# Performance work log

Hardware: AMD Instinct MI355X
Metric: run time of the kernel (lower is better)

## Reference

```python
import jax, jax.numpy as jnp
import numpy as np

N, E, D, H, ED = 50000, 400000, 64, 4, 16
C = D  # out_channels per head (GATv2Conv(model_dim, model_dim, ...))


def setup_inputs() -> dict:
    key = jax.random.key(0)
    ks = jax.random.split(key, 24)
    sD = 1.0 / np.sqrt(D)
    sE = 1.0 / np.sqrt(ED)
    sC = 1.0 / np.sqrt(C)
    inp = {
        "h": jax.random.normal(ks[0], (N, D), jnp.float32),
        "edge_index": jax.random.randint(ks[1], (2, E), 0, N, dtype=jnp.int32),
        "edge_attr": jax.random.normal(ks[2], (E, ED), jnp.float32),
    }
    for i, name in enumerate(["g1", "g2"]):
        b = 3 + i * 9
        inp[f"{name}_Wl"] = jax.random.normal(ks[b], (D, H * C), jnp.float32) * sD
        inp[f"{name}_bl"] = jax.random.normal(ks[b + 1], (H * C,), jnp.float32) * 0.02
        inp[f"{name}_Wr"] = jax.random.normal(ks[b + 2], (D, H * C), jnp.float32) * sD
        inp[f"{name}_br"] = jax.random.normal(ks[b + 3], (H * C,), jnp.float32) * 0.02
        inp[f"{name}_We"] = jax.random.normal(ks[b + 4], (ED, H * C), jnp.float32) * sE
        inp[f"{name}_att"] = jax.random.normal(ks[b + 5], (H, C), jnp.float32) * sC
        inp[f"{name}_bias"] = jax.random.normal(ks[b + 6], (C,), jnp.float32) * 0.02
        inp[f"ln{i+1}_g"] = jnp.ones((D,), jnp.float32)
        inp[f"ln{i+1}_b"] = jnp.zeros((D,), jnp.float32)
    return inp


def _layer_norm(x, g, b):
    mu = jnp.mean(x, axis=-1, keepdims=True)
    var = jnp.mean((x - mu) ** 2, axis=-1, keepdims=True)
    return (x - mu) * jax.lax.rsqrt(var + 1e-5) * g + b


def _gatv2(h, src, dst, edge_attr, Wl, bl, Wr, br, We, att, bias):
    # PyG GATv2Conv, concat=False, negative_slope=0.2, aggregation at dst
    xl = (h @ Wl + bl).reshape(N, H, C)  # source transform
    xr = (h @ Wr + br).reshape(N, H, C)  # target transform
    ez = (edge_attr @ We).reshape(E, H, C)
    x = jax.nn.leaky_relu(xl[src] + xr[dst] + ez, negative_slope=0.2)  # [E,H,C]
    alpha = jnp.einsum('ehc,hc->eh', x, att)  # attention logits per edge/head
    amax = jax.ops.segment_max(alpha, dst, num_segments=N)
    amax = jnp.where(jnp.isfinite(amax), amax, 0.0)
    ex = jnp.exp(alpha - amax[dst])
    denom = jax.ops.segment_sum(ex, dst, num_segments=N)
    a = ex / (denom[dst] + 1e-16)  # segment softmax over incoming edges
    out = jax.ops.segment_sum(xl[src] * a[..., None], dst, num_segments=N)  # [N,H,C]
    return jnp.mean(out, axis=1) + bias  # concat=False -> head mean, then bias


def reference(h, edge_index, edge_attr,
              g1_Wl, g1_bl, g1_Wr, g1_br, g1_We, g1_att, g1_bias, ln1_g, ln1_b,
              g2_Wl, g2_bl, g2_Wr, g2_br, g2_We, g2_att, g2_bias, ln2_g, ln2_b):
    src, dst = edge_index[0], edge_index[1]
    identity = h
    x = _gatv2(h, src, dst, edge_attr, g1_Wl, g1_bl, g1_Wr, g1_br, g1_We, g1_att, g1_bias)
    x = jax.nn.gelu(_layer_norm(x, ln1_g, ln1_b), approximate=False)
    x = _gatv2(x, src, dst, edge_attr, g2_Wl, g2_bl, g2_Wr, g2_br, g2_We, g2_att, g2_bias)
    x = _layer_norm(x, ln2_g, ln2_b)
    return jax.nn.gelu(x + identity, approximate=False)
```

## Files before the change

kernel.cpp:

```cpp
#include <hip/hip_runtime.h>
#include <math.h>

#define NN  50000
#define EE  400000
#define DD  64
#define HH  4
#define HC  256
#define EDD 16

typedef _Float16 half_t;
typedef _Float16 h2 __attribute__((ext_vector_type(2)));

__device__ __forceinline__ float gelu_exact(float x) {
    return 0.5f * x * (1.0f + erff(x * 0.70710678118654752440f));
}
__device__ __forceinline__ float fast_exp(float x) {
    return __builtin_amdgcn_exp2f(x * 1.44269504088896340736f);
}

template <int CTRL>
__device__ __forceinline__ float dpp_add(float x) {
    const int t = __builtin_amdgcn_update_dpp(0, __float_as_int(x), CTRL, 0xF, 0xF, true);
    return x + __int_as_float(t);
}
__device__ __forceinline__ float row_sum16(float x) {
    x = dpp_add<0x128>(x);
    x = dpp_add<0x124>(x);
    x = dpp_add<0x122>(x);
    x = dpp_add<0x121>(x);
    return x;
}

__global__ void fill_u32(unsigned* __restrict__ p, unsigned v, int n) {
    int i = blockIdx.x * blockDim.x + threadIdx.x;
    int s = gridDim.x * blockDim.x;
    for (; i < n; i += s) p[i] = v;
}

__global__ void hist_k(const int* __restrict__ ei, int* __restrict__ deg) {
    int e = blockIdx.x * 256 + threadIdx.x;
    if (e < EE) atomicAdd(&deg[ei[EE + e]], 1);
}
__global__ void scan1_k(const int* __restrict__ deg, int* __restrict__ rowptr,
                        int* __restrict__ bsum) {
    __shared__ int s[256];
    int t = threadIdx.x, i = blockIdx.x * 256 + t;
    int v = (i < NN) ? deg[i] : 0;
    s[t] = v; __syncthreads();
    for (int o = 1; o < 256; o <<= 1) {
        int u = (t >= o) ? s[t - o] : 0;
        __syncthreads();
        s[t] += u;
        __syncthreads();
    }
    if (i < NN) rowptr[i] = s[t] - v;
    if (t == 255) bsum[blockIdx.x] = s[255];
}
__global__ void scan2_k(int* __restrict__ bsum, int nb) {
    __shared__ int s[256];
    int t = threadIdx.x;
    int v = (t < nb) ? bsum[t] : 0;
    s[t] = v; __syncthreads();
    for (int o = 1; o < 256; o <<= 1) {
        int u = (t >= o) ? s[t - o] : 0;
        __syncthreads();
        s[t] += u;
        __syncthreads();
    }
    if (t < nb) bsum[t] = s[t] - v;
}
__global__ void scan3_k(int* __restrict__ rowptr, const int* __restrict__ bsum,
                        int* __restrict__ cursor) {
    int i = blockIdx.x * 256 + threadIdx.x;
    if (i < NN) {
        int r = rowptr[i] + bsum[blockIdx.x];
        rowptr[i] = r;
        cursor[i] = r;
    }
    if (i == 0) rowptr[NN] = EE;
}
__global__ void scatter_k(const int* __restrict__ ei, int* __restrict__ cursor,
                          const float* __restrict__ ea,
                          int* __restrict__ srcs, half_t* __restrict__ ea_h) {
    int e = blockIdx.x * 256 + threadIdx.x;
    if (e >= EE) return;
    int dst = ei[EE + e];
    int pos = atomicAdd(&cursor[dst], 1);
    srcs[pos] = ei[e];
    const float* s = ea + (long)e * EDD;
    half_t tmp[EDD];
#pragma unroll
    for (int k = 0; k < EDD; k++) tmp[k] = (half_t)s[k];
    int4* d = (int4*)(ea_h + (long)pos * EDD);
    d[0] = *(const int4*)&tmp[0];
    d[1] = *(const int4*)&tmp[8];
}

__global__ void wrange_k(const int* __restrict__ rowptr, int* __restrict__ wstart,
                         int* __restrict__ srcs, int nw, int cpe) {
    int w = blockIdx.x * 256 + threadIdx.x;
    if (blockIdx.x == 0 && threadIdx.x < 16) srcs[EE + threadIdx.x] = 0;
    if (w > nw) return;
    if (w == nw) { wstart[nw] = NN; return; }
    const int lo = w * cpe;
    int l = 0, r = NN;
    while (l < r) { int m = (l + r) >> 1; if (rowptr[m] >= lo) r = m; else l = m + 1; }
    wstart[w] = l;
}

__global__ __launch_bounds__(256) void gemm_node_lr(
    const float* __restrict__ X,
    const float* __restrict__ Wl, const float* __restrict__ bl,
    const float* __restrict__ Wr, const float* __restrict__ br,
    float* __restrict__ Yl, float* __restrict__ Yr)
{
    __shared__ half_t xs[32][64];
    const int tid  = threadIdx.x;
    const int col  = tid;
    const int base = blockIdx.x * 32;

#pragma unroll
    for (int i = 0; i < 2; i++) {
        const int f   = tid + i * 256;
        const int r   = f >> 4;
        const int row = base + r;
        const int rr  = (row < NN) ? row : (NN - 1);
        const float4 v = *(const float4*)(X + (long)rr * 64 + ((f & 15) << 2));
        h2 p0; p0.x = (half_t)v.x; p0.y = (half_t)v.y;
        h2 p1; p1.x = (half_t)v.z; p1.y = (half_t)v.w;
        int2 w;
        w.x = __builtin_bit_cast(int, p0);
        w.y = __builtin_bit_cast(int, p1);
        *(int2*)&xs[r][(f & 15) << 2] = w;
    }

    int wlp[32], wrp[32];
#pragma unroll
    for (int kk = 0; kk < 32; kk++) {
        h2 a;
        a.x = (half_t)Wl[(2 * kk)     * 256 + col];
        a.y = (half_t)Wl[(2 * kk + 1) * 256 + col];
        wlp[kk] = __builtin_bit_cast(int, a);
        h2 b;
        b.x = (half_t)Wr[(2 * kk)     * 256 + col];
        b.y = (half_t)Wr[(2 * kk + 1) * 256 + col];
        wrp[kk] = __builtin_bit_cast(int, b);
    }
    const float bbl = bl[col];
    const float bbr = br[col];

    __syncthreads();

#pragma unroll 2
    for (int r = 0; r < 32; r++) {
        const int row = base + r;
        float l0 = 0.f, l1 = 0.f, l2 = 0.f, l3 = 0.f;
        float r0 = 0.f, r1 = 0.f, r2 = 0.f, r3 = 0.f;
#pragma unroll
        for (int q = 0; q < 8; q++) {
            const int4 blk = *(const int4*)&xs[r][q << 3];
            const int* pr = (const int*)&blk;
            l0 = __builtin_amdgcn_fdot2(__builtin_bit_cast(h2, pr[0]),
                                        __builtin_bit_cast(h2, wlp[q * 4 + 0]), l0, false);
            l1 = __builtin_amdgcn_fdot2(__builtin_bit_cast(h2, pr[1]),
                                        __builtin_bit_cast(h2, wlp[q * 4 + 1]), l1, false);
            l2 = __builtin_amdgcn_fdot2(__builtin_bit_cast(h2, pr[2]),
                                        __builtin_bit_cast(h2, wlp[q * 4 + 2]), l2, false);
            l3 = __builtin_amdgcn_fdot2(__builtin_bit_cast(h2, pr[3]),
                                        __builtin_bit_cast(h2, wlp[q * 4 + 3]), l3, false);
            r0 = __builtin_amdgcn_fdot2(__builtin_bit_cast(h2, pr[0]),
                                        __builtin_bit_cast(h2, wrp[q * 4 + 0]), r0, false);
            r1 = __builtin_amdgcn_fdot2(__builtin_bit_cast(h2, pr[1]),
                                        __builtin_bit_cast(h2, wrp[q * 4 + 1]), r1, false);
            r2 = __builtin_amdgcn_fdot2(__builtin_bit_cast(h2, pr[2]),
                                        __builtin_bit_cast(h2, wrp[q * 4 + 2]), r2, false);
            r3 = __builtin_amdgcn_fdot2(__builtin_bit_cast(h2, pr[3]),
                                        __builtin_bit_cast(h2, wrp[q * 4 + 3]), r3, false);
        }
        if (row < NN) {
            Yl[(long)row * 256 + col] = (l0 + l1) + (l2 + l3) + bbl;
            Yr[(long)row * 256 + col] = (r0 + r1) + (r2 + r3) + bbr;
        }
    }
}

__device__ __forceinline__ float edge_part_dot2(const h2 ev[8], const int wpk[8][4],
                                                const float4 xlv, const float4 xrv,
                                                const float4 a4) {
    float e0 = 0.f, e1 = 0.f, e2 = 0.f, e3 = 0.f;
#pragma unroll
    for (int k = 0; k < 8; k++) {
        e0 = __builtin_amdgcn_fdot2(ev[k], __builtin_bit_cast(h2, wpk[k][0]), e0, false);
        e1 = __builtin_amdgcn_fdot2(ev[k], __builtin_bit_cast(h2, wpk[k][1]), e1, false);
        e2 = __builtin_amdgcn_fdot2(ev[k], __builtin_bit_cast(h2, wpk[k][2]), e2, false);
        e3 = __builtin_amdgcn_fdot2(ev[k], __builtin_bit_cast(h2, wpk[k][3]), e3, false);
    }
    float s0 = xlv.x + xrv.x + e0;
    float s1 = xlv.y + xrv.y + e1;
    float s2 = xlv.z + xrv.z + e2;
    float s3 = xlv.w + xrv.w + e3;
    s0 = (s0 > 0.f) ? s0 : 0.2f * s0;
    s1 = (s1 > 0.f) ? s1 : 0.2f * s1;
    s2 = (s2 > 0.f) ? s2 : 0.2f * s2;
    s3 = (s3 > 0.f) ? s3 : 0.2f * s3;
    return fmaf(s0, a4.x, fmaf(s1, a4.y, fmaf(s2, a4.z, s3 * a4.w)));
}

__global__ __launch_bounds__(256, 4) void fused_edge_node_k(
    const int* __restrict__ wstart,
    const int* __restrict__ rowptr, const int* __restrict__ srcs,
    const half_t* __restrict__ ea_h,
    const float* __restrict__ We, const float* __restrict__ att,
    const float* __restrict__ xl, const float* __restrict__ xr,
    const float* __restrict__ bias, const float* __restrict__ lng,
    const float* __restrict__ lnb, const float* __restrict__ identity,
    float* __restrict__ x1out, float* __restrict__ outp, int mode)
{
    const int lane = threadIdx.x & 63;
    const int h    = lane >> 4;
    const int jj   = lane & 15;
    const int gc   = (h << 6) + (jj << 2);
    const int c    = (jj << 2) + h;

    int wpk[8][4];
#pragma unroll
    for (int kk = 0; kk < 8; kk++) {
#pragma unroll
        for (int j = 0; j < 4; j++) {
            h2 t;
            t.x = (half_t)We[(2 * kk)     * HC + gc + j];
            t.y = (half_t)We[(2 * kk + 1) * HC + gc + j];
            wpk[kk][j] = __builtin_bit_cast(int, t);
        }
    }
#pragma unroll
    for (int kk = 0; kk < 8; kk++)
#pragma unroll
        for (int j = 0; j < 4; j++) asm volatile("" : "+v"(wpk[kk][j]));

    const float4 a4 = *(const float4*)(att + gc);
    const float bb  = bias[c];
    const float gg  = lng[c];
    const float cc  = lnb[c];

    const int wid  = blockIdx.x * 4 + (threadIdx.x >> 6);
    const int nbeg = __builtin_amdgcn_readfirstlane(wstart[wid]);
    const int nend = __builtin_amdgcn_readfirstlane(wstart[wid + 1]);

    int p0v = rowptr[nbeg];
    int p1v = rowptr[nbeg + 1];
    int sAn = srcs[p0v];
    int sBn = srcs[p0v + 1];

    for (int n = nbeg; n < nend; n++) {
        const int p0 = __builtin_amdgcn_readfirstlane(p0v);
        const int p1 = __builtin_amdgcn_readfirstlane(p1v);
        p0v = p1;
        p1v = rowptr[(n + 2 <= NN) ? (n + 2) : NN];
        int sA = sAn, sB = sBn;
        sAn = srcs[p1];
        sBn = srcs[p1 + 1];

        const float4 xrv = *(const float4*)(xr + (long)n * HC + gc);

        float dsum = 0.f;
        float ac0 = 0.f, ac1 = 0.f, ac2 = 0.f, ac3 = 0.f;

        int p = p0;
        for (; p + 1 < p1; p += 2) {
            const int srcA = __builtin_amdgcn_readfirstlane(sA);
            const int srcB = __builtin_amdgcn_readfirstlane(sB);
            sA = srcs[p + 2];
            sB = srcs[p + 3];

            const float4 xA = *(const float4*)(xl + (long)srcA * HC + gc);
            const float4 xB = *(const float4*)(xl + (long)srcB * HC + gc);

            const int4* __restrict__ e16 = (const int4*)(ea_h + (long)p * EDD);
            h2 evA[8], evB[8];
            *(int4*)&evA[0] = e16[0];  *(int4*)&evA[4] = e16[1];
            *(int4*)&evB[0] = e16[2];  *(int4*)&evB[4] = e16[3];

            float ptA = edge_part_dot2(evA, wpk, xA, xrv, a4);
            float ptB = edge_part_dot2(evB, wpk, xB, xrv, a4);

            ptA = row_sum16(ptA);
            ptB = row_sum16(ptB);

            const float wA = fast_exp(ptA);
            const float wB = fast_exp(ptB);
            dsum += (wA + wB);
            ac0 = fmaf(wA, xA.x, ac0); ac1 = fmaf(wA, xA.y, ac1);
            ac2 = fmaf(wA, xA.z, ac2); ac3 = fmaf(wA, xA.w, ac3);
            ac0 = fmaf(wB, xB.x, ac0); ac1 = fmaf(wB, xB.y, ac1);
            ac2 = fmaf(wB, xB.z, ac2); ac3 = fmaf(wB, xB.w, ac3);
        }

        if (p < p1) {
            const int src = __builtin_amdgcn_readfirstlane(sA);
            const float4 xv = *(const float4*)(xl + (long)src * HC + gc);
            const int4* __restrict__ e16 = (const int4*)(ea_h + (long)p * EDD);
            h2 ev[8];
            *(int4*)&ev[0] = e16[0];  *(int4*)&ev[4] = e16[1];
            float pt = edge_part_dot2(ev, wpk, xv, xrv, a4);
            pt = row_sum16(pt);
            const float w = fast_exp(pt);
            dsum += w;
            ac0 = fmaf(w, xv.x, ac0); ac1 = fmaf(w, xv.y, ac1);
            ac2 = fmaf(w, xv.z, ac2); ac3 = fmaf(w, xv.w, ac3);
        }

        const float inv = 1.0f / (dsum + 1e-16f);
        float v0 = ac0 * inv, v1 = ac1 * inv, v2 = ac2 * inv, v3 = ac3 * inv;

        v0 += __shfl_xor(v0, 16, 64); v0 += __shfl_xor(v0, 32, 64);
        v1 += __shfl_xor(v1, 16, 64); v1 += __shfl_xor(v1, 32, 64);
        v2 += __shfl_xor(v2, 16, 64); v2 += __shfl_xor(v2, 32, 64);
        v3 += __shfl_xor(v3, 16, 64); v3 += __shfl_xor(v3, 32, 64);

        float vv = (h == 0) ? v0 : (h == 1) ? v1 : (h == 2) ? v2 : v3;
        vv = vv * 0.25f + bb;

        float s = row_sum16(vv);
        s += __shfl_xor(s, 16, 64); s += __shfl_xor(s, 32, 64);
        const float mu = s * (1.0f / 64.0f);
        const float d  = vv - mu;
        float qv = row_sum16(d * d);
        qv += __shfl_xor(qv, 16, 64); qv += __shfl_xor(qv, 32, 64);
        const float rs = rsqrtf(qv * (1.0f / 64.0f) + 1e-5f);

        const float y = d * rs * gg + cc;
        if (mode == 0) {
            x1out[(long)n * DD + c] = gelu_exact(y);
        } else {
            const float id = identity[(long)n * DD + c];
            outp[(long)n * DD + c] = gelu_exact(y + id);
        }
    }
}

extern "C" void kernel_launch(void* const* d_in, const int* in_sizes, int n_in,
                              void* d_out, int out_size, void* d_ws, size_t ws_size,
                              hipStream_t stream) {
    (void)in_sizes; (void)n_in; (void)out_size; (void)ws_size;

    const float* h     = (const float*)d_in[0];
    const int*   ei    = (const int*)d_in[1];
    const float* ea    = (const float*)d_in[2];
    const float* g1Wl  = (const float*)d_in[3];
    const float* g1bl  = (const float*)d_in[4];
    const float* g1Wr  = (const float*)d_in[5];
    const float* g1br  = (const float*)d_in[6];
    const float* g1We  = (const float*)d_in[7];
    const float* g1att = (const float*)d_in[8];
    const float* g1bias= (const float*)d_in[9];
    const float* ln1g  = (const float*)d_in[10];
    const float* ln1b  = (const float*)d_in[11];
    const float* g2Wl  = (const float*)d_in[12];
    const float* g2bl  = (const float*)d_in[13];
    const float* g2Wr  = (const float*)d_in[14];
    const float* g2br  = (const float*)d_in[15];
    const float* g2We  = (const float*)d_in[16];
    const float* g2att = (const float*)d_in[17];
    const float* g2bias= (const float*)d_in[18];
    const float* ln2g  = (const float*)d_in[19];
    const float* ln2b  = (const float*)d_in[20];

    float* out = (float*)d_out;

    const int FUSED_BLOCKS = 4096;
    const int NW  = FUSED_BLOCKS * 4;
    const int CPE = (EE + NW - 1) / NW;

    float* ws = (float*)d_ws;
    size_t o = 0;
    float* xl     = ws + o;         o += 12800000;
    float* xr     = ws + o;         o += 12800000;
    float* x1     = ws + o;         o += 3200000;
    int*   rowptr = (int*)(ws + o); o += 50004;
    int*   deg    = (int*)(ws + o); o += 50000;
    int*   cursor = (int*)(ws + o); o += 50000;
    int*   bsum   = (int*)(ws + o); o += 256;
    int*   srcs   = (int*)(ws + o); o += 400016;
    int*   wstart = (int*)(ws + o); o += NW + 8;
    half_t* ea_h  = (half_t*)(ws + o); o += 3200064;

    const int GEMM_BLOCKS  = (NN + 31) / 32;
    const int SCAN_BLOCKS  = (NN + 255) / 256;
    const int EDGE_BLOCKS  = (EE + 255) / 256;
    const int WR_BLOCKS    = (NW + 1 + 255) / 256;

    fill_u32<<<256, 256, 0, stream>>>((unsigned*)deg, 0u, NN);
    hist_k<<<EDGE_BLOCKS, 256, 0, stream>>>(ei, deg);
    scan1_k<<<SCAN_BLOCKS, 256, 0, stream>>>(deg, rowptr, bsum);
    scan2_k<<<1, 256, 0, stream>>>(bsum, SCAN_BLOCKS);
    scan3_k<<<SCAN_BLOCKS, 256, 0, stream>>>(rowptr, bsum, cursor);
    wrange_k<<<WR_BLOCKS, 256, 0, stream>>>(rowptr, wstart, srcs, NW, CPE);
    scatter_k<<<EDGE_BLOCKS, 256, 0, stream>>>(ei, cursor, ea, srcs, ea_h);

    gemm_node_lr<<<GEMM_BLOCKS, 256, 0, stream>>>(h, g1Wl, g1bl, g1Wr, g1br, xl, xr);
    fused_edge_node_k<<<FUSED_BLOCKS, 256, 0, stream>>>(wstart, rowptr, srcs, ea_h,
                                                        g1We, g1att, xl, xr,
                                                        g1bias, ln1g, ln1b,
                                                        h, x1, out, 0);

    gemm_node_lr<<<GEMM_BLOCKS, 256, 0, stream>>>(x1, g2Wl, g2bl, g2Wr, g2br, xl, xr);
    fused_edge_node_k<<<FUSED_BLOCKS, 256, 0, stream>>>(wstart, rowptr, srcs, ea_h,
                                                        g2We, g2att, xl, xr,
                                                        g2bias, ln2g, ln2b,
                                                        h, x1, out, 1);
}
```

Before: 404.7 us.

## Stage per-wave edge attributes in LDS and merge scan kernels

After: 404.8 us. About the same (+0.0%).

```diff
diff --git a/kernel.cpp b/kernel.cpp
--- a/kernel.cpp
+++ b/kernel.cpp
@@ -7,6 +7,7 @@
 #define HH  4
 #define HC  256
 #define EDD 16
+#define CAPE 96
 
 typedef _Float16 half_t;
 typedef _Float16 h2 __attribute__((ext_vector_type(2)));
@@ -56,7 +57,8 @@
     if (i < NN) rowptr[i] = s[t] - v;
     if (t == 255) bsum[blockIdx.x] = s[255];
 }
-__global__ void scan2_k(int* __restrict__ bsum, int nb) {
+__global__ void scan3_k(int* __restrict__ rowptr, const int* __restrict__ bsum,
+                        int* __restrict__ cursor, int nb) {
     __shared__ int s[256];
     int t = threadIdx.x;
     int v = (t < nb) ? bsum[t] : 0;
@@ -67,13 +69,10 @@
         s[t] += u;
         __syncthreads();
     }
-    if (t < nb) bsum[t] = s[t] - v;
-}
-__global__ void scan3_k(int* __restrict__ rowptr, const int* __restrict__ bsum,
-                        int* __restrict__ cursor) {
-    int i = blockIdx.x * 256 + threadIdx.x;
+    const int add = (blockIdx.x > 0) ? s[blockIdx.x - 1] : 0;
+    int i = blockIdx.x * 256 + t;
     if (i < NN) {
-        int r = rowptr[i] + bsum[blockIdx.x];
+        int r = rowptr[i] + add;
         rowptr[i] = r;
         cursor[i] = r;
     }
@@ -216,11 +215,13 @@
     const float* __restrict__ lnb, const float* __restrict__ identity,
     float* __restrict__ x1out, float* __restrict__ outp, int mode)
 {
-    const int lane = threadIdx.x & 63;
-    const int h    = lane >> 4;
-    const int jj   = lane & 15;
-    const int gc   = (h << 6) + (jj << 2);
-    const int c    = (jj << 2) + h;
+    __shared__ int4 eabuf[4][CAPE * 2];
+    const int lane  = threadIdx.x & 63;
+    const int wslot = threadIdx.x >> 6;
+    const int h     = lane >> 4;
+    const int jj    = lane & 15;
+    const int gc    = (h << 6) + (jj << 2);
+    const int c     = (jj << 2) + h;
 
     int wpk[8][4];
 #pragma unroll
@@ -243,9 +244,19 @@
     const float gg  = lng[c];
     const float cc  = lnb[c];
 
-    const int wid  = blockIdx.x * 4 + (threadIdx.x >> 6);
+    const int wid  = blockIdx.x * 4 + wslot;
     const int nbeg = __builtin_amdgcn_readfirstlane(wstart[wid]);
     const int nend = __builtin_amdgcn_readfirstlane(wstart[wid + 1]);
+
+    const int estart = __builtin_amdgcn_readfirstlane(rowptr[nbeg]);
+    const int eend   = __builtin_amdgcn_readfirstlane(rowptr[nend]);
+    {
+        int nstage = eend - estart;
+        if (nstage > CAPE) nstage = CAPE;
+        const int4* __restrict__ gsrc = (const int4*)(ea_h + (long)estart * EDD);
+        int4* l4 = &eabuf[wslot][0];
+        for (int i = lane; i < nstage * 2; i += 64) l4[i] = gsrc[i];
+    }
 
     int p0v = rowptr[nbeg];
     int p1v = rowptr[nbeg + 1];
@@ -276,10 +287,12 @@
             const float4 xA = *(const float4*)(xl + (long)srcA * HC + gc);
             const float4 xB = *(const float4*)(xl + (long)srcB * HC + gc);
 
-            const int4* __restrict__ e16 = (const int4*)(ea_h + (long)p * EDD);
+            int idx = p - estart;
+            if (idx > CAPE - 2) idx = CAPE - 2;
+            const int4* __restrict__ e4 = &eabuf[wslot][idx * 2];
             h2 evA[8], evB[8];
-            *(int4*)&evA[0] = e16[0];  *(int4*)&evA[4] = e16[1];
-            *(int4*)&evB[0] = e16[2];  *(int4*)&evB[4] = e16[3];
+            *(int4*)&evA[0] = e4[0];  *(int4*)&evA[4] = e4[1];
+            *(int4*)&evB[0] = e4[2];  *(int4*)&evB[4] = e4[3];
 
             float ptA = edge_part_dot2(evA, wpk, xA, xrv, a4);
             float ptB = edge_part_dot2(evB, wpk, xB, xrv, a4);
@@ -299,9 +312,11 @@
         if (p < p1) {
             const int src = __builtin_amdgcn_readfirstlane(sA);
             const float4 xv = *(const float4*)(xl + (long)src * HC + gc);
-            const int4* __restrict__ e16 = (const int4*)(ea_h + (long)p * EDD);
+            int idx = p - estart;
+            if (idx > CAPE - 1) idx = CAPE - 1;
+            const int4* __restrict__ e4 = &eabuf[wslot][idx * 2];
             h2 ev[8];
-            *(int4*)&ev[0] = e16[0];  *(int4*)&ev[4] = e16[1];
+            *(int4*)&ev[0] = e4[0];  *(int4*)&ev[4] = e4[1];
             float pt = edge_part_dot2(ev, wpk, xv, xrv, a4);
             pt = row_sum16(pt);
             const float w = fast_exp(pt);
@@ -393,8 +408,7 @@
     fill_u32<<<256, 256, 0, stream>>>((unsigned*)deg, 0u, NN);
     hist_k<<<EDGE_BLOCKS, 256, 0, stream>>>(ei, deg);
     scan1_k<<<SCAN_BLOCKS, 256, 0, stream>>>(deg, rowptr, bsum);
-    scan2_k<<<1, 256, 0, stream>>>(bsum, SCAN_BLOCKS);
-    scan3_k<<<SCAN_BLOCKS, 256, 0, stream>>>(rowptr, bsum, cursor);
+    scan3_k<<<SCAN_BLOCKS, 256, 0, stream>>>(rowptr, bsum, cursor, SCAN_BLOCKS);
     wrange_k<<<WR_BLOCKS, 256, 0, stream>>>(rowptr, wstart, srcs, NW, CPE);
     scatter_k<<<EDGE_BLOCKS, 256, 0, stream>>>(ei, cursor, ea, srcs, ea_h);
 
```
